# Kernel tuning notes

Measured on AMD Instinct MI355X. Metric: run time of the kernel, lower is better.

The kernel has to match this reference:

```python
import math
import jax, jax.numpy as jnp
import numpy as np

B, I, G, C, D = 8192, 512, 32, 16, 32  # batch, dim_input, groups, num_components, dim_output
CD = C * D


def setup_inputs() -> dict:
    key = jax.random.key(0)
    ks = jax.random.split(key, 8)
    bound = 1.0 / math.sqrt(I)

    def unif(k, shape):
        return jax.random.uniform(k, shape, jnp.float32, -bound, bound)

    x = jax.random.normal(ks[0], (B, I), jnp.float32)
    # soft group-mixture weights (rows sum to 1, as produced upstream)
    g = jax.nn.softmax(jax.random.normal(ks[1], (B, G), jnp.float32), axis=-1)
    return {
        "x": x,
        "g": g,
        "W_mu": unif(ks[2], (G, I, CD)),
        "b_mu": unif(ks[3], (G, CD)),
        "W_sigma": unif(ks[4], (G, I, CD)),
        "b_sigma": unif(ks[5], (G, CD)),
        "W_pi": unif(ks[6], (G, I, C)),
        "b_pi": unif(ks[7], (G, C)),
    }


def _group_linear(x, g, W, b):
    # Fused form of: w_b = (g @ W.reshape(G, I*O)).reshape(B, I, O); x[:,None,:] @ w_b + g @ b
    # einsum avoids materializing the [B, I, O] per-sample weight tensor.
    return jnp.einsum("bi,gio,bg->bo", x, W, g) + g @ b


def reference(x, g, W_mu, b_mu, W_sigma, b_sigma, W_pi, b_pi):
    logits = _group_linear(x, g, W_pi, b_pi)                      # [B, C]
    loc = _group_linear(x, g, W_mu, b_mu)                         # [B, C*D]
    scale = jax.nn.softplus(_group_linear(x, g, W_sigma, b_sigma)) + 1e-7  # [B, C*D]
    # GroupGMM returns a MixtureSameFamily parameterized by (logits, loc, scale);
    # we return the concatenated parameter tensor [B, C + 2*C*D].
    return jnp.concatenate([logits, loc, scale], axis=-1)
```

## Files before the change

### kernel.cpp

```cpp
#include <hip/hip_runtime.h>
#include <hip/hip_bf16.h>

#define BATCH 8192
#define IDIM  512
#define GDIM  32
#define NOUT  1040
#define NPAD  1152
#define KW    16384
#define BM    128
#define BN    128
#define KQ    128

typedef short bf16x8 __attribute__((ext_vector_type(8)));
typedef float floatx4 __attribute__((ext_vector_type(4)));

__device__ inline unsigned pk2(float a, float b) {
    union { __hip_bfloat162 h2; unsigned u; } cv;
    cv.h2 = __float22bfloat162_rn(float2{a, b});
    return cv.u;
}

__global__ void cvt_bf16(const float* __restrict__ s, unsigned short* __restrict__ d) {
    int t = blockIdx.x * 256 + threadIdx.x;
    const float4* sp = (const float4*)s + (size_t)t * 2;
    float4 a = sp[0], b = sp[1];
    uint4 p;
    p.x = pk2(a.x, a.y); p.y = pk2(a.z, a.w);
    p.z = pk2(b.x, b.y); p.w = pk2(b.z, b.w);
    *(uint4*)(d + (size_t)t * 8) = p;
}

__global__ void prep_wt(const float* __restrict__ Wmu, const float* __restrict__ Wsig,
                        const float* __restrict__ Wpi, unsigned short* __restrict__ Wt) {
    int n = blockIdx.y * 256 + threadIdx.x;
    if (n >= NPAD) return;
    int k0 = blockIdx.x * 8;
    float v[8];
#pragma unroll
    for (int j = 0; j < 8; ++j) {
        int k = k0 + j, gg = k >> 9, i = k & 511;
        float val = 0.0f;
        if (n < 16)         val = Wpi [(gg * 512 + i) * 16  + n];
        else if (n < 528)   val = Wmu [(gg * 512 + i) * 512 + (n - 16)];
        else if (n < NOUT)  val = Wsig[(gg * 512 + i) * 512 + (n - 528)];
        v[j] = val;
    }
    uint4 p;
    p.x = pk2(v[0], v[1]); p.y = pk2(v[2], v[3]);
    p.z = pk2(v[4], v[5]); p.w = pk2(v[6], v[7]);
    const int col = n >> 7, r = n & 127;
    const int h = r >> 6, tn = (r >> 4) & 3, l15 = r & 15;
    const int kk = k0 >> 5, q = (k0 >> 3) & 3;
    size_t idx = ((size_t)(col * 512 + kk) << 12) + ((((h * 4 + tn) * 4 + q) * 16 + l15) * 8);
    *(uint4*)&Wt[idx] = p;
}

__global__ void prep_wb(const float* __restrict__ bmu, const float* __restrict__ bsig,
                        const float* __restrict__ bpi, unsigned short* __restrict__ Wb) {
    int n = blockIdx.y * 256 + threadIdx.x;
    if (n >= NPAD) return;
    int k0 = blockIdx.x * 8;
    float v[8];
#pragma unroll
    for (int j = 0; j < 8; ++j) {
        int gg = k0 + j;
        float val = 0.0f;
        if (n < 16)         val = bpi [gg * 16  + n];
        else if (n < 528)   val = bmu [gg * 512 + (n - 16)];
        else if (n < NOUT)  val = bsig[gg * 512 + (n - 528)];
        v[j] = val;
    }
    uint4 p;
    p.x = pk2(v[0], v[1]); p.y = pk2(v[2], v[3]);
    p.z = pk2(v[4], v[5]); p.w = pk2(v[6], v[7]);
    *(uint4*)&Wb[(size_t)n * GDIM + k0] = p;
}

__global__ __launch_bounds__(256, 2) void gemm_gmm(
        const unsigned short* __restrict__ xb, const unsigned short* __restrict__ gb,
        const float* __restrict__ g, const unsigned short* __restrict__ Wt,
        const unsigned short* __restrict__ Wb, float* __restrict__ out) {
    __shared__ unsigned short lA[BM * KQ];
    __shared__ float gsc[GDIM * BM];

    const int t = threadIdx.x, lane = t & 63, w = t >> 6;
    const int wm = (w & 1) * 64, wn = (w >> 1) * 64;
    const int q = lane >> 4, l15 = lane & 15;

    const int bx = blockIdx.x;
    const int seq = (bx & 7) * 72 + (bx >> 3);
    const int col = seq >> 6, mblk = seq & 63;
    const int m0 = mblk * BM, n0 = col * BN;

#pragma unroll
    for (int j = 0; j < 16; ++j) {
        int idx = t + 256 * j;
        int gg = idx >> 7, row = idx & 127;
        gsc[idx] = g[(size_t)(m0 + row) * GDIM + gg];
    }

    const unsigned short* Bbase = Wt + ((size_t)col * 512 << 12)
                                + (((wn >> 6) * 256 + lane) * 8);

    floatx4 acc[4][4] = {};
    floatx4 P[4][4] = {};
    uint4 breg[2][4];
    const int swA = l15 & 7;

    auto loadB = [&](int kk, int slot) {
        const unsigned kg = (((kk >> 2) & 31) * 16) + ((kk >> 7) * 4) + (kk & 3);
        const unsigned short* p = Bbase + ((size_t)kg << 12);
#pragma unroll
        for (int tn = 0; tn < 4; ++tn)
            breg[slot][tn] = *(const uint4*)(p + tn * 512);
    };

    loadB(0, 0);
    for (int kb = 0; kb < 4; ++kb) {
        __syncthreads();
        {
            const int r = t >> 1;
            const unsigned short* src = xb + (size_t)(m0 + r) * IDIM + kb * KQ + (t & 1) * 64;
#pragma unroll
            for (int j = 0; j < 8; ++j) {
                int gi = (t & 1) * 8 + j;
                uint4 v = *(const uint4*)(src + j * 8);
                *(uint4*)&lA[(r * 16 + (gi ^ (r & 7))) * 8] = v;
            }
        }
        __syncthreads();

        for (int gg = 0; gg < GDIM; ++gg) {
#pragma unroll
            for (int ks = 0; ks < 4; ++ks) {
                const int kk = ((kb * GDIM + gg) << 2) + ks;
                if (kk + 1 < 512) loadB(kk + 1, (kk + 1) & 1);
                bf16x8 af[4];
#pragma unroll
                for (int tm = 0; tm < 4; ++tm)
                    af[tm] = *(const bf16x8*)
                        &lA[((wm + tm * 16 + l15) * 16 + ((ks * 4 + q) ^ swA)) * 8];
                const int slot = kk & 1;
#pragma unroll
                for (int tm = 0; tm < 4; ++tm)
#pragma unroll
                    for (int tn = 0; tn < 4; ++tn)
                        P[tm][tn] = __builtin_amdgcn_mfma_f32_16x16x32_bf16(
                            af[tm], *(const bf16x8*)&breg[slot][tn], P[tm][tn], 0, 0, 0);
            }
#pragma unroll
            for (int tm = 0; tm < 4; ++tm) {
                floatx4 s4 = *(const floatx4*)&gsc[gg * BM + wm + tm * 16 + q * 4];
#pragma unroll
                for (int tn = 0; tn < 4; ++tn) {
#pragma unroll
                    for (int r = 0; r < 4; ++r)
                        acc[tm][tn][r] += s4[r] * P[tm][tn][r];
                    P[tm][tn] = (floatx4){0.f, 0.f, 0.f, 0.f};
                }
            }
        }
    }

    __syncthreads();
    {
        const int r = t >> 1;
        const unsigned short* src = gb + (size_t)(m0 + r) * GDIM + (t & 1) * 16;
        *(uint4*)&lA[r * 40 + (t & 1) * 16]     = *(const uint4*)(src);
        *(uint4*)&lA[r * 40 + (t & 1) * 16 + 8] = *(const uint4*)(src + 8);
    }
    __syncthreads();
    {
        bf16x8 afb[4], bb[4];
#pragma unroll
        for (int tm = 0; tm < 4; ++tm)
            afb[tm] = *(const bf16x8*)&lA[(wm + tm * 16 + l15) * 40 + q * 8];
#pragma unroll
        for (int tn = 0; tn < 4; ++tn)
            bb[tn] = *(const bf16x8*)(Wb + (size_t)(n0 + wn + tn * 16 + l15) * GDIM + q * 8);
#pragma unroll
        for (int tm = 0; tm < 4; ++tm)
#pragma unroll
            for (int tn = 0; tn < 4; ++tn)
                acc[tm][tn] = __builtin_amdgcn_mfma_f32_16x16x32_bf16(
                    afb[tm], bb[tn], acc[tm][tn], 0, 0, 0);
    }

#pragma unroll
    for (int tn = 0; tn < 4; ++tn) {
        int n = n0 + wn + tn * 16 + l15;
        if (n >= NOUT) continue;
        bool is_scale = (n >= 528);
#pragma unroll
        for (int tm = 0; tm < 4; ++tm) {
            int mbase = m0 + wm + tm * 16 + q * 4;
#pragma unroll
            for (int r = 0; r < 4; ++r) {
                float vv = acc[tm][tn][r];
                if (is_scale) {
                    float sp = (vv > 15.0f) ? vv : log1pf(expf(vv));
                    vv = sp + 1e-7f;
                }
                out[(size_t)(mbase + r) * NOUT + n] = vv;
            }
        }
    }
}

extern "C" void kernel_launch(void* const* d_in, const int* in_sizes, int n_in,
                              void* d_out, int out_size, void* d_ws, size_t ws_size,
                              hipStream_t stream) {
    const float* x    = (const float*)d_in[0];
    const float* g    = (const float*)d_in[1];
    const float* Wmu  = (const float*)d_in[2];
    const float* bmu  = (const float*)d_in[3];
    const float* Wsig = (const float*)d_in[4];
    const float* bsig = (const float*)d_in[5];
    const float* Wpi  = (const float*)d_in[6];
    const float* bpi  = (const float*)d_in[7];
    float* out = (float*)d_out;

    char* ws = (char*)d_ws;
    unsigned short* Wt = (unsigned short*)ws;  ws += (size_t)NPAD * KW * 2;
    unsigned short* xb = (unsigned short*)ws;  ws += (size_t)BATCH * IDIM * 2;
    unsigned short* gb = (unsigned short*)ws;  ws += (size_t)BATCH * GDIM * 2;
    unsigned short* Wb = (unsigned short*)ws;

    cvt_bf16<<<BATCH * IDIM / 2048, 256, 0, stream>>>(x, xb);
    cvt_bf16<<<BATCH * GDIM / 2048, 256, 0, stream>>>(g, gb);
    prep_wt<<<dim3(KW / 8, 5), 256, 0, stream>>>(Wmu, Wsig, Wpi, Wt);
    prep_wb<<<dim3(GDIM / 8, 5), 256, 0, stream>>>(bmu, bsig, bpi, Wb);
    gemm_gmm<<<(BATCH / BM) * (NPAD / BN), 256, 0, stream>>>(xb, gb, g, Wt, Wb, out);
}
```

Baseline: 562.6 us.

## Fold group weights into accumulator via running ratio rescaling, deepen B prefetch

Drops the per-group partial accumulator P and its scaled-add epilogue. Before each group the kernel now multiplies the main accumulator by g[prev]/g[cur] (precomputed in LDS), accumulates the MFMAs directly into it, and multiplies by g[31] once at the end. This frees about 64 accumulator registers and removes the per-group zeroing and FMA pass, and the freed registers pay for a B-operand prefetch three steps ahead across four register slots. The cost is a division by g, which assumes every g entry is nonzero and can lose precision when g values are very small.

```diff
diff --git a/kernel.cpp b/kernel.cpp
--- a/kernel.cpp
+++ b/kernel.cpp
@@ -81,7 +81,8 @@
         const float* __restrict__ g, const unsigned short* __restrict__ Wt,
         const unsigned short* __restrict__ Wb, float* __restrict__ out) {
     __shared__ unsigned short lA[BM * KQ];
-    __shared__ float gsc[GDIM * BM];
+    __shared__ float ratL[GDIM * BM];
+    __shared__ float g31L[BM];
 
     const int t = threadIdx.x, lane = t & 63, w = t >> 6;
     const int wm = (w & 1) * 64, wn = (w >> 1) * 64;
@@ -92,30 +93,41 @@
     const int col = seq >> 6, mblk = seq & 63;
     const int m0 = mblk * BM, n0 = col * BN;
 
+    const unsigned short* Bbase = Wt + ((size_t)col * 512 << 12)
+                                + (((wn >> 6) * 256 + lane) * 8);
+
+    floatx4 acc[4][4] = {};
+    uint4 breg[4][4];
+    floatx4 r4[4];
+    const int swA = l15 & 7;
+
+    auto loadB = [&](int kk, int slot) {
+        const unsigned kg = (((kk >> 2) & 31) * 16) + ((kk >> 7) * 4) + (kk & 3);
+        const unsigned short* p = Bbase + ((size_t)kg << 12);
+#pragma unroll
+        for (int tn = 0; tn < 4; ++tn)
+            breg[slot][tn] = *(const uint4*)(p + tn * 512);
+    };
+    auto loadR = [&](int gg) {
+#pragma unroll
+        for (int tm = 0; tm < 4; ++tm)
+            r4[tm] = *(const floatx4*)&ratL[gg * BM + wm + tm * 16 + q * 4];
+    };
+
+    loadB(0, 0); loadB(1, 1); loadB(2, 2);
+
 #pragma unroll
     for (int j = 0; j < 16; ++j) {
         int idx = t + 256 * j;
         int gg = idx >> 7, row = idx & 127;
-        gsc[idx] = g[(size_t)(m0 + row) * GDIM + gg];
-    }
-
-    const unsigned short* Bbase = Wt + ((size_t)col * 512 << 12)
-                                + (((wn >> 6) * 256 + lane) * 8);
-
-    floatx4 acc[4][4] = {};
-    floatx4 P[4][4] = {};
-    uint4 breg[2][4];
-    const int swA = l15 & 7;
-
-    auto loadB = [&](int kk, int slot) {
-        const unsigned kg = (((kk >> 2) & 31) * 16) + ((kk >> 7) * 4) + (kk & 3);
-        const unsigned short* p = Bbase + ((size_t)kg << 12);
-#pragma unroll
-        for (int tn = 0; tn < 4; ++tn)
-            breg[slot][tn] = *(const uint4*)(p + tn * 512);
-    };
-
-    loadB(0, 0);
+        float cur  = g[(size_t)(m0 + row) * GDIM + gg];
+        float prev = g[(size_t)(m0 + row) * GDIM + ((gg + 31) & 31)];
+        ratL[idx] = prev / cur;
+    }
+    if (t < BM) g31L[t] = g[(size_t)(m0 + t) * GDIM + 31];
+    __syncthreads();
+    loadR(0);
+
     for (int kb = 0; kb < 4; ++kb) {
         __syncthreads();
         {
@@ -132,34 +144,41 @@
 
         for (int gg = 0; gg < GDIM; ++gg) {
 #pragma unroll
+            for (int tm = 0; tm < 4; ++tm)
+#pragma unroll
+                for (int tn = 0; tn < 4; ++tn)
+#pragma unroll
+                    for (int r = 0; r < 4; ++r)
+                        acc[tm][tn][r] *= r4[tm][r];
+            loadR((gg + 1) & 31);
+
+#pragma unroll
             for (int ks = 0; ks < 4; ++ks) {
                 const int kk = ((kb * GDIM + gg) << 2) + ks;
-                if (kk + 1 < 512) loadB(kk + 1, (kk + 1) & 1);
+                if (kk + 3 < 512) loadB(kk + 3, (ks + 3) & 3);
                 bf16x8 af[4];
 #pragma unroll
                 for (int tm = 0; tm < 4; ++tm)
                     af[tm] = *(const bf16x8*)
                         &lA[((wm + tm * 16 + l15) * 16 + ((ks * 4 + q) ^ swA)) * 8];
-                const int slot = kk & 1;
 #pragma unroll
                 for (int tm = 0; tm < 4; ++tm)
 #pragma unroll
                     for (int tn = 0; tn < 4; ++tn)
-                        P[tm][tn] = __builtin_amdgcn_mfma_f32_16x16x32_bf16(
-                            af[tm], *(const bf16x8*)&breg[slot][tn], P[tm][tn], 0, 0, 0);
-            }
-#pragma unroll
-            for (int tm = 0; tm < 4; ++tm) {
-                floatx4 s4 = *(const floatx4*)&gsc[gg * BM + wm + tm * 16 + q * 4];
-#pragma unroll
-                for (int tn = 0; tn < 4; ++tn) {
-#pragma unroll
-                    for (int r = 0; r < 4; ++r)
-                        acc[tm][tn][r] += s4[r] * P[tm][tn][r];
-                    P[tm][tn] = (floatx4){0.f, 0.f, 0.f, 0.f};
-                }
+                        acc[tm][tn] = __builtin_amdgcn_mfma_f32_16x16x32_bf16(
+                            af[tm], *(const bf16x8*)&breg[ks][tn], acc[tm][tn], 0, 0, 0);
             }
         }
+    }
+
+#pragma unroll
+    for (int tm = 0; tm < 4; ++tm) {
+        floatx4 gl = *(const floatx4*)&g31L[wm + tm * 16 + q * 4];
+#pragma unroll
+        for (int tn = 0; tn < 4; ++tn)
+#pragma unroll
+            for (int r = 0; r < 4; ++r)
+                acc[tm][tn][r] *= gl[r];
     }
 
     __syncthreads();
```

New measurement: 509.0 us. 9.5% less time.
